# Performance work log

Hardware: AMD Instinct MI355X
Metric: run time of the kernel (lower is better)

## Reference

```python
import jax, jax.numpy as jnp
import numpy as np

B, NCAMS = 1, 6
C_FEAT = 64                     # fusion_feat_in_dim
H, W = 88, 160                  # per-camera feature map size at fusion level
VOX_SIZE = (100, 100, 20)       # (x_dim, y_dim, z_dim) voxel counts
VOX_STR = (-50.0, -50.0, -15.0)
VOX_UNIT = (1.0, 1.0, 1.5)
N_VOX = VOX_SIZE[0] * VOX_SIZE[1] * VOX_SIZE[2]
EPS = 1e-8
V_PRE = 64                      # voxel_pre_dim[0]


def make_voxel_pts(dtype):
    # [B, 4, N]; homogeneous (x, y, z, 1) points, layout [z, y, x] flattened
    xs = jnp.linspace(VOX_STR[0], VOX_STR[0] + VOX_UNIT[0] * (VOX_SIZE[0] - 1), VOX_SIZE[0], dtype=dtype)
    ys = jnp.linspace(VOX_STR[1], VOX_STR[1] + VOX_UNIT[1] * (VOX_SIZE[1] - 1), VOX_SIZE[1], dtype=dtype)
    zs = jnp.linspace(VOX_STR[2], VOX_STR[2] + VOX_UNIT[2] * (VOX_SIZE[2] - 1), VOX_SIZE[2], dtype=dtype)
    zdim, ydim, xdim = VOX_SIZE[2], VOX_SIZE[1], VOX_SIZE[0]
    gx = jnp.broadcast_to(xs[None, None, :], (zdim, ydim, xdim)).reshape(-1)
    gy = jnp.broadcast_to(ys[None, :, None], (zdim, ydim, xdim)).reshape(-1)
    gz = jnp.broadcast_to(zs[:, None, None], (zdim, ydim, xdim)).reshape(-1)
    pts = jnp.stack([gx, gy, gz, jnp.ones_like(gx)], axis=0)  # [4, N]
    return jnp.broadcast_to(pts[None], (B, 4, N_VOX))


def _gather(imgf, iy, ix, Wd):
    # imgf: [BN, C, H*W]; iy/ix: [BN, N] int32 -> [BN, C, N]
    lin = iy * Wd + ix
    return jnp.take_along_axis(imgf, lin[:, None, :], axis=2)


def bilinear_sample(img, gx, gy):
    # grid_sample(mode='bilinear', padding_mode='zeros', align_corners=True)
    BN, C, Hd, Wd = img.shape
    x = (gx + 1.0) * 0.5 * (Wd - 1)
    y = (gy + 1.0) * 0.5 * (Hd - 1)
    x0 = jnp.floor(x); y0 = jnp.floor(y)
    wx1 = x - x0; wx0 = 1.0 - wx1
    wy1 = y - y0; wy0 = 1.0 - wy1
    imgf = img.reshape(BN, C, Hd * Wd)
    out = jnp.zeros((BN, C, gx.shape[1]), dtype=img.dtype)
    for xi, wxi in ((x0, wx0), (x0 + 1.0, wx1)):
        for yi, wyi in ((y0, wy0), (y0 + 1.0, wy1)):
            valid = (xi >= 0) & (xi <= Wd - 1) & (yi >= 0) & (yi <= Hd - 1)
            ii = jnp.clip(xi, 0, Wd - 1).astype(jnp.int32)
            jj = jnp.clip(yi, 0, Hd - 1).astype(jnp.int32)
            w = (wxi * wyi * valid.astype(img.dtype))[:, None, :]
            out = out + _gather(imgf, jj, ii, Wd) * w
    return out


def nearest_sample(img, gx, gy):
    # grid_sample(mode='nearest', padding_mode='zeros', align_corners=True)
    BN, C, Hd, Wd = img.shape
    x = (gx + 1.0) * 0.5 * (Wd - 1)
    y = (gy + 1.0) * 0.5 * (Hd - 1)
    xi = jnp.round(x); yi = jnp.round(y)
    valid = (xi >= 0) & (xi <= Wd - 1) & (yi >= 0) & (yi <= Hd - 1)
    ii = jnp.clip(xi, 0, Wd - 1).astype(jnp.int32)
    jj = jnp.clip(yi, 0, Hd - 1).astype(jnp.int32)
    imgf = img.reshape(BN, C, Hd * Wd)
    return _gather(imgf, jj, ii, Wd) * valid[:, None, :].astype(img.dtype)


def setup_inputs() -> dict:
    key = jax.random.key(0)
    ks = jax.random.split(key, 8)
    return {
        'multi_img_feat': jax.random.normal(ks[0], (B, NCAMS, C_FEAT, H, W), jnp.float32),
        'mask': jax.random.uniform(ks[1], (B, NCAMS, 1, H, W), jnp.float32),
        'K': jax.random.normal(ks[2], (B, NCAMS, 4, 4), jnp.float32),
        'extrinsics': jax.random.normal(ks[3], (B, NCAMS, 4, 4), jnp.float32),
        'w_no': jax.random.normal(ks[4], (V_PRE, C_FEAT + 1), jnp.float32) * 0.05,
        'b_no': jax.random.normal(ks[5], (V_PRE,), jnp.float32) * 0.05,
        'w_o': jax.random.normal(ks[6], (V_PRE, 2 * (C_FEAT + 1)), jnp.float32) * 0.05,
        'b_o': jax.random.normal(ks[7], (V_PRE,), jnp.float32) * 0.05,
    }


def reference(multi_img_feat, mask, K, extrinsics, w_no, b_no, w_o, b_o):
    Bb, NC, C, Hd, Wd = multi_img_feat.shape
    dt = multi_img_feat.dtype
    vpts = make_voxel_pts(dt)                                          # [B,4,N]
    vpts_c = jnp.broadcast_to(vpts[:, None], (Bb, NC, 4, N_VOX)).reshape(Bb * NC, 4, N_VOX)
    feats = multi_img_feat.reshape(Bb * NC, C, Hd, Wd)
    masks = mask.reshape(Bb * NC, 1, Hd, Wd)                           # interp to (H,W) is identity (same size, align_corners)
    ext = extrinsics.reshape(Bb * NC, 4, 4)[:, :3, :]
    K3 = K.reshape(Bb * NC, 4, 4)[:, :3, :3]

    v_local = jnp.einsum('bij,bjn->bin', ext, vpts_c)                  # [BN,3,N]
    cam_pts = jnp.einsum('bij,bjn->bin', K3, v_local)
    pix = cam_pts[:, :2] / (cam_pts[:, 2:3] + EPS)
    pix = jnp.where(jnp.all(jnp.isfinite(pix)), pix, jnp.clip(pix, -Wd * 2.0, Wd * 2.0))
    gx = (pix[:, 0] / (Wd - 1) - 0.5) * 2.0                            # [BN,N] normalized coords
    gy = (pix[:, 1] / (Hd - 1) - 0.5) * 2.0

    feat_w = bilinear_sample(feats, gx, gy)                            # [BN,C,N]
    m_occ = nearest_sample(masks, gx, gy) > 0.5                        # [BN,1,N]
    m_depth = v_local[:, 2:3] > 0
    oob = (gx > 1) | (gx < -1) | (gy > 1) | (gy < -1)
    valid = (m_occ & m_depth & (~oob)[:, None, :]).astype(dt)          # [BN,1,N]

    feat_w = jnp.concatenate([feat_w, v_local[:, 2:3] / VOX_SIZE[0]], axis=1) * valid  # [BN,C+1,N]

    feat_w = feat_w.reshape(Bb, NC, C + 1, N_VOX)
    valid = valid.reshape(Bb, NC, 1, N_VOX)
    count = valid.sum(axis=1)                                          # [B,1,N]

    # non-overlap branch: voxels seen by exactly one camera
    no_mask = (count == 1).astype(dt)
    vox_no = feat_w.sum(axis=1) * no_mask
    vox_no = jax.nn.elu(jnp.einsum('oc,bcn->bon', w_no, vox_no) + b_no[None, :, None]) * no_mask

    # overlap branch: cams {0,3,4} vs {1,2,5}
    o_mask = (count == 2).astype(dt)
    feat1 = feat_w[:, 0] + feat_w[:, 3] + feat_w[:, 4]
    feat2 = feat_w[:, 1] + feat_w[:, 2] + feat_w[:, 5]
    vox_o = jnp.concatenate([feat1, feat2], axis=1)                    # [B,2*(C+1),N]
    vox_o = jax.nn.elu(jnp.einsum('oc,bcn->bon', w_o, vox_o) + b_o[None, :, None]) * o_mask

    return vox_no + vox_o                                              # [B, V_PRE, N]
```

## Files before the change

### kernel.cpp

```cpp
#include <hip/hip_runtime.h>
#include <cmath>

#define NC 6
#define CF 64
#define HH 88
#define WW 160
#define NPIX 14080
#define NVOX 200000
#define VPRE 64
#define VB 128
#define NTH 512
#define NWV 8

typedef unsigned int u32;

__global__ __launch_bounds__(256) void zfill(float4* __restrict__ out, int n4) {
    int i = blockIdx.x * 256 + threadIdx.x;
    int stride = gridDim.x * 256;
    for (; i < n4; i += stride) out[i] = make_float4(0.f, 0.f, 0.f, 0.f);
}

__global__ __launch_bounds__(256) void transpose_feats(const float* __restrict__ in,
                                                       float* __restrict__ out) {
    __shared__ float tile[64 * 65];
    int blk = blockIdx.x;
    int c = blk / 220;
    int p0 = (blk - c * 220) * 64;
    int tid = threadIdx.x;
    int lane = tid & 63;
    int quad = tid >> 6;
    for (int r = quad; r < 64; r += 4)
        tile[r * 65 + lane] = in[(c * 64 + r) * NPIX + p0 + lane];
    __syncthreads();
    for (int r = quad; r < 64; r += 4)
        out[((c * NPIX) + p0 + r) * 64 + lane] = tile[lane * 65 + r];
}

__device__ __forceinline__ float elu1(float x) { return x > 0.0f ? x : expm1f(x); }

__device__ __forceinline__ float gather_bilin(const float* __restrict__ fsrc, int useT,
                                              int lane, int cam, float x, float y) {
    float x0f = floorf(x), y0f = floorf(y);
    float wx1 = x - x0f, wx0 = 1.0f - wx1;
    float wy1 = y - y0f, wy0 = 1.0f - wy1;
    float x1f = x0f + 1.0f, y1f = y0f + 1.0f;
    float bx0 = (x0f >= 0.0f && x0f <= 159.0f) ? 1.0f : 0.0f;
    float bx1 = (x1f >= 0.0f && x1f <= 159.0f) ? 1.0f : 0.0f;
    float by0 = (y0f >= 0.0f && y0f <= 87.0f) ? 1.0f : 0.0f;
    float by1 = (y1f >= 0.0f && y1f <= 87.0f) ? 1.0f : 0.0f;
    int ix0 = (int)fminf(fmaxf(x0f, 0.0f), 159.0f);
    int ix1 = (int)fminf(fmaxf(x1f, 0.0f), 159.0f);
    int iy0 = (int)fminf(fmaxf(y0f, 0.0f), 87.0f);
    int iy1 = (int)fminf(fmaxf(y1f, 0.0f), 87.0f);
    int A = useT ? 64 : 1;
    int Boff = useT ? (cam * NPIX * 64 + lane) : ((cam * 64 + lane) * NPIX);
    float v00 = fsrc[(iy0 * WW + ix0) * A + Boff];
    float v01 = fsrc[(iy1 * WW + ix0) * A + Boff];
    float v10 = fsrc[(iy0 * WW + ix1) * A + Boff];
    float v11 = fsrc[(iy1 * WW + ix1) * A + Boff];
    float fv;
    fv  = (wx0 * wy0 * bx0 * by0) * v00;
    fv += (wx0 * wy1 * bx0 * by1) * v01;
    fv += (wx1 * wy0 * bx1 * by0) * v10;
    fv += (wx1 * wy1 * bx1 * by1) * v11;
    return fv;
}

#define FMA8_STEP(W0,W1,W2,W3,W4,W5,W6,W7,CG,F0,F1,F2,F3) \
    a0 += W0[CG]*F0; a0 += W0[CG+1]*F1; a0 += W0[CG+2]*F2; a0 += W0[CG+3]*F3; \
    a1 += W1[CG]*F0; a1 += W1[CG+1]*F1; a1 += W1[CG+2]*F2; a1 += W1[CG+3]*F3; \
    a2 += W2[CG]*F0; a2 += W2[CG+1]*F1; a2 += W2[CG+2]*F2; a2 += W2[CG+3]*F3; \
    a3 += W3[CG]*F0; a3 += W3[CG+1]*F1; a3 += W3[CG+2]*F2; a3 += W3[CG+3]*F3; \
    a4 += W4[CG]*F0; a4 += W4[CG+1]*F1; a4 += W4[CG+2]*F2; a4 += W4[CG+3]*F3; \
    a5 += W5[CG]*F0; a5 += W5[CG+1]*F1; a5 += W5[CG+2]*F2; a5 += W5[CG+3]*F3; \
    a6 += W6[CG]*F0; a6 += W6[CG+1]*F1; a6 += W6[CG+2]*F2; a6 += W6[CG+3]*F3; \
    a7 += W7[CG]*F0; a7 += W7[CG+1]*F1; a7 += W7[CG+2]*F2; a7 += W7[CG+3]*F3;

__global__ __launch_bounds__(NTH, 4) void vox_main(
    const float* __restrict__ feats,
    const float* __restrict__ featT,
    const float* __restrict__ mask,
    const float* __restrict__ Kg,
    const float* __restrict__ ext,
    const float* __restrict__ wno,
    const float* __restrict__ bno,
    const float* __restrict__ wo,
    const float* __restrict__ bo,
    float* __restrict__ outp,
    int useT)
{
    __shared__ float s_ext[72];
    __shared__ float s_K[54];
    __shared__ __align__(16) float4 s_pair[NC * VB];
    __shared__ float s_F[65 * 66];
    __shared__ u32 s_list1[VB], s_list2[VB];
    __shared__ int s_n1, s_n2;

    int tid = threadIdx.x;
    int lane = tid & 63;
    int wv = tid >> 6;
    int base = blockIdx.x * VB;

    if (tid == 0) { s_n1 = 0; s_n2 = 0; }
    if (tid >= 64 && tid < 136) {
        int i = tid - 64;
        s_ext[i] = ext[(i / 12) * 16 + (i % 12)];
    }
    if (tid >= 192 && tid < 246) {
        int i = tid - 192; int cam = i / 9; int e = i - cam * 9;
        s_K[i] = Kg[cam * 16 + (e / 3) * 4 + (e % 3)];
    }
    __syncthreads();

    for (int p = tid; p < NC * VB; p += NTH) {
        #pragma clang fp contract(off)
        int cam = p >> 7;
        int v = p & (VB - 1);
        int n = base + v;
        if (n < NVOX) {
            int xi = n % 100;
            int t = n / 100;
            int yi = t % 100;
            int zi = t / 100;
            float X = -50.0f + (float)xi;
            float Y = -50.0f + (float)yi;
            float Z = -15.0f + 1.5f * (float)zi;
            const float* E = s_ext + cam * 12;
            const float* Kk = s_K + cam * 9;
            float vl0 = E[0]*X + E[1]*Y + E[2]*Z + E[3];
            float vl1 = E[4]*X + E[5]*Y + E[6]*Z + E[7];
            float vl2 = E[8]*X + E[9]*Y + E[10]*Z + E[11];
            float c0 = Kk[0]*vl0 + Kk[1]*vl1 + Kk[2]*vl2;
            float c1 = Kk[3]*vl0 + Kk[4]*vl1 + Kk[5]*vl2;
            float c2 = Kk[6]*vl0 + Kk[7]*vl1 + Kk[8]*vl2;
            float pz = c2 + 1e-8f;
            float px = c0 / pz;
            float py = c1 / pz;
            float gx = (px / 159.0f - 0.5f) * 2.0f;
            float gy = (py / 87.0f - 0.5f) * 2.0f;
            float x = ((gx + 1.0f) * 0.5f) * 159.0f;
            float y = ((gy + 1.0f) * 0.5f) * 87.0f;
            float xr = rintf(x), yr = rintf(y);
            bool nv = (xr >= 0.0f) && (xr <= 159.0f) && (yr >= 0.0f) && (yr <= 87.0f);
            float mval = 0.0f;
            if (nv) mval = mask[(cam * HH + (int)yr) * WW + (int)xr];
            bool ok = (mval > 0.5f) && (vl2 > 0.0f) &&
                      !((gx > 1.0f) || (gx < -1.0f) || (gy > 1.0f) || (gy < -1.0f));
            s_pair[cam * VB + v] = make_float4(x, y, vl2, ok ? 1.0f : 0.0f);
        } else {
            s_pair[cam * VB + v] = make_float4(0.0f, 0.0f, 0.0f, 0.0f);
        }
    }
    __syncthreads();

    if (tid < VB) {
        int v = tid;
        const float* pw = (const float*)s_pair;
        int cnt = 0, cam0 = 0, cam1 = 0;
        #pragma unroll
        for (int c = 0; c < NC; ++c) {
            float w = pw[(c * VB + v) * 4 + 3];
            if (w != 0.0f) { if (cnt == 0) cam0 = c; else if (cnt == 1) cam1 = c; ++cnt; }
        }
        if (cnt == 1) {
            int s = atomicAdd(&s_n1, 1);
            s_list1[s] = (u32)(v | (cam0 << 8));
        } else if (cnt == 2) {
            int s = atomicAdd(&s_n2, 1);
            s_list2[s] = (u32)(v | (cam0 << 8) | (cam1 << 12));
        }
    }
    __syncthreads();

    int n1 = s_n1, n2 = s_n2;
    const float* fsrc = useT ? featT : feats;
    int wvu = __builtin_amdgcn_readfirstlane(wv);
    int obase = wvu * 8;
    const float* w0n = wno + (obase + 0) * 65;
    const float* w1n = wno + (obase + 1) * 65;
    const float* w2n = wno + (obase + 2) * 65;
    const float* w3n = wno + (obase + 3) * 65;
    const float* w4n = wno + (obase + 4) * 65;
    const float* w5n = wno + (obase + 5) * 65;
    const float* w6n = wno + (obase + 6) * 65;
    const float* w7n = wno + (obase + 7) * 65;
    const float* w0o = wo + (obase + 0) * 130;
    const float* w1o = wo + (obase + 1) * 130;
    const float* w2o = wo + (obase + 2) * 130;
    const float* w3o = wo + (obase + 3) * 130;
    const float* w4o = wo + (obase + 4) * 130;
    const float* w5o = wo + (obase + 5) * 130;
    const float* w6o = wo + (obase + 6) * 130;
    const float* w7o = wo + (obase + 7) * 130;

    for (int t0 = 0; t0 < n1; t0 += 64) {
        int tl = min(64, n1 - t0);
        for (int e = wv; e < tl; e += NWV) {
            u32 ent = s_list1[t0 + e];
            int v = ent & 127, c = (ent >> 8) & 7;
            float4 pd = s_pair[c * VB + v];
            float fv = gather_bilin(fsrc, useT, lane, c, pd.x, pd.y);
            s_F[lane * 66 + e] = fv;
            if (lane == 0) s_F[64 * 66 + e] = pd.z / 100.0f;
        }
        __syncthreads();
        float a0 = bno[obase + 0], a1 = bno[obase + 1], a2 = bno[obase + 2], a3 = bno[obase + 3];
        float a4 = bno[obase + 4], a5 = bno[obase + 5], a6 = bno[obase + 6], a7 = bno[obase + 7];
        for (int cg = 0; cg < 64; cg += 4) {
            float f0 = s_F[(cg + 0) * 66 + lane];
            float f1 = s_F[(cg + 1) * 66 + lane];
            float f2 = s_F[(cg + 2) * 66 + lane];
            float f3 = s_F[(cg + 3) * 66 + lane];
            FMA8_STEP(w0n, w1n, w2n, w3n, w4n, w5n, w6n, w7n, cg, f0, f1, f2, f3)
        }
        float fd = s_F[64 * 66 + lane];
        a0 += w0n[64] * fd; a1 += w1n[64] * fd; a2 += w2n[64] * fd; a3 += w3n[64] * fd;
        a4 += w4n[64] * fd; a5 += w5n[64] * fd; a6 += w6n[64] * fd; a7 += w7n[64] * fd;
        if (lane < tl) {
            size_t col = (size_t)(base + (int)(s_list1[t0 + lane] & 127));
            outp[(size_t)(obase + 0) * NVOX + col] = elu1(a0);
            outp[(size_t)(obase + 1) * NVOX + col] = elu1(a1);
            outp[(size_t)(obase + 2) * NVOX + col] = elu1(a2);
            outp[(size_t)(obase + 3) * NVOX + col] = elu1(a3);
            outp[(size_t)(obase + 4) * NVOX + col] = elu1(a4);
            outp[(size_t)(obase + 5) * NVOX + col] = elu1(a5);
            outp[(size_t)(obase + 6) * NVOX + col] = elu1(a6);
            outp[(size_t)(obase + 7) * NVOX + col] = elu1(a7);
        }
        __syncthreads();
    }

    for (int t0 = 0; t0 < n2; t0 += 64) {
        int tl = min(64, n2 - t0);
        for (int e = wv; e < tl; e += NWV) {
            u32 ent = s_list2[t0 + e];
            int v = ent & 127;
            int c0 = (ent >> 8) & 15, c1 = (ent >> 12) & 15;
            float fg = 0.0f, dd = 0.0f;
            if (!(c0 == 1 || c0 == 2 || c0 == 5)) {
                float4 pd = s_pair[c0 * VB + v];
                fg += gather_bilin(fsrc, useT, lane, c0, pd.x, pd.y);
                dd += pd.z / 100.0f;
            }
            if (!(c1 == 1 || c1 == 2 || c1 == 5)) {
                float4 pd = s_pair[c1 * VB + v];
                fg += gather_bilin(fsrc, useT, lane, c1, pd.x, pd.y);
                dd += pd.z / 100.0f;
            }
            s_F[lane * 66 + e] = fg;
            if (lane == 0) s_F[64 * 66 + e] = dd;
        }
        __syncthreads();
        float a0 = bo[obase + 0], a1 = bo[obase + 1], a2 = bo[obase + 2], a3 = bo[obase + 3];
        float a4 = bo[obase + 4], a5 = bo[obase + 5], a6 = bo[obase + 6], a7 = bo[obase + 7];
        for (int cg = 0; cg < 64; cg += 4) {
            float f0 = s_F[(cg + 0) * 66 + lane];
            float f1 = s_F[(cg + 1) * 66 + lane];
            float f2 = s_F[(cg + 2) * 66 + lane];
            float f3 = s_F[(cg + 3) * 66 + lane];
            FMA8_STEP(w0o, w1o, w2o, w3o, w4o, w5o, w6o, w7o, cg, f0, f1, f2, f3)
        }
        {
            float fd = s_F[64 * 66 + lane];
            a0 += w0o[64] * fd; a1 += w1o[64] * fd; a2 += w2o[64] * fd; a3 += w3o[64] * fd;
            a4 += w4o[64] * fd; a5 += w5o[64] * fd; a6 += w6o[64] * fd; a7 += w7o[64] * fd;
        }
        __syncthreads();
        for (int e = wv; e < tl; e += NWV) {
            u32 ent = s_list2[t0 + e];
            int v = ent & 127;
            int c0 = (ent >> 8) & 15, c1 = (ent >> 12) & 15;
            float fg = 0.0f, dd = 0.0f;
            if (c0 == 1 || c0 == 2 || c0 == 5) {
                float4 pd = s_pair[c0 * VB + v];
                fg += gather_bilin(fsrc, useT, lane, c0, pd.x, pd.y);
                dd += pd.z / 100.0f;
            }
            if (c1 == 1 || c1 == 2 || c1 == 5) {
                float4 pd = s_pair[c1 * VB + v];
                fg += gather_bilin(fsrc, useT, lane, c1, pd.x, pd.y);
                dd += pd.z / 100.0f;
            }
            s_F[lane * 66 + e] = fg;
            if (lane == 0) s_F[64 * 66 + e] = dd;
        }
        __syncthreads();
        for (int cg = 0; cg < 64; cg += 4) {
            float f0 = s_F[(cg + 0) * 66 + lane];
            float f1 = s_F[(cg + 1) * 66 + lane];
            float f2 = s_F[(cg + 2) * 66 + lane];
            float f3 = s_F[(cg + 3) * 66 + lane];
            int cgo = cg + 65;
            FMA8_STEP(w0o, w1o, w2o, w3o, w4o, w5o, w6o, w7o, cgo, f0, f1, f2, f3)
        }
        {
            float fd = s_F[64 * 66 + lane];
            a0 += w0o[129] * fd; a1 += w1o[129] * fd; a2 += w2o[129] * fd; a3 += w3o[129] * fd;
            a4 += w4o[129] * fd; a5 += w5o[129] * fd; a6 += w6o[129] * fd; a7 += w7o[129] * fd;
        }
        if (lane < tl) {
            size_t col = (size_t)(base + (int)(s_list2[t0 + lane] & 127));
            outp[(size_t)(obase + 0) * NVOX + col] = elu1(a0);
            outp[(size_t)(obase + 1) * NVOX + col] = elu1(a1);
            outp[(size_t)(obase + 2) * NVOX + col] = elu1(a2);
            outp[(size_t)(obase + 3) * NVOX + col] = elu1(a3);
            outp[(size_t)(obase + 4) * NVOX + col] = elu1(a4);
            outp[(size_t)(obase + 5) * NVOX + col] = elu1(a5);
            outp[(size_t)(obase + 6) * NVOX + col] = elu1(a6);
            outp[(size_t)(obase + 7) * NVOX + col] = elu1(a7);
        }
        __syncthreads();
    }
}

extern "C" void kernel_launch(void* const* d_in, const int* in_sizes, int n_in,
                              void* d_out, int out_size, void* d_ws, size_t ws_size,
                              hipStream_t stream) {
    const float* feats = (const float*)d_in[0];
    const float* mask  = (const float*)d_in[1];
    const float* Kg    = (const float*)d_in[2];
    const float* ext   = (const float*)d_in[3];
    const float* wno   = (const float*)d_in[4];
    const float* bno   = (const float*)d_in[5];
    const float* wo    = (const float*)d_in[6];
    const float* bo    = (const float*)d_in[7];
    float* outp = (float*)d_out;
    float* featT = (float*)d_ws;

    int n4 = out_size / 4;
    zfill<<<2048, 256, 0, stream>>>((float4*)d_out, n4);

    size_t need = (size_t)NC * CF * NPIX * sizeof(float);
    int useT = (ws_size >= need) ? 1 : 0;
    if (useT) {
        transpose_feats<<<NC * 220, 256, 0, stream>>>(feats, featT);
    }
    int nblk = (NVOX + VB - 1) / VB;
    vox_main<<<nblk, NTH, 0, stream>>>(feats, featT, mask, Kg, ext,
                                       wno, bno, wo, bo, outp, useT);
}
```

Measured before the change: 165.8 us.

## Split voxel kernel into geometry compaction pass and dense matvec pass

Adds a prep kernel that projects voxels, classifies them by camera count, and compacts the single-camera and two-camera voxels into global record lists using atomic counters. A second persistent kernel then processes full 64-voxel tiles of these lists for the gather and matvec, so tiles are no longer mostly empty as they were with per-block sparse voxels. This costs an extra launch and a round trip of records through the workspace. The new path is taken only when the workspace is large enough, otherwise the old fused kernel is used.

Measured after the change: 187.8 us. +13.3%, slower.

```diff
diff --git a/kernel.cpp b/kernel.cpp
--- a/kernel.cpp
+++ b/kernel.cpp
@@ -14,10 +14,20 @@
 
 typedef unsigned int u32;
 
-__global__ __launch_bounds__(256) void zfill(float4* __restrict__ out, int n4) {
+#define FEATT_BYTES  (6u * 64u * 14080u * 4u)
+#define REC1_OFF     FEATT_BYTES
+#define REC1_BYTES   (200000u * 16u)
+#define REC2_OFF     (REC1_OFF + REC1_BYTES)
+#define REC2_BYTES   (200000u * 16u)
+#define CNT_OFF      (REC2_OFF + REC2_BYTES)
+#define WS_NEED      (CNT_OFF + 16u)
+
+__global__ __launch_bounds__(256) void zfill(float4* __restrict__ out, int n4,
+                                             int* __restrict__ cnt) {
     int i = blockIdx.x * 256 + threadIdx.x;
     int stride = gridDim.x * 256;
     for (; i < n4; i += stride) out[i] = make_float4(0.f, 0.f, 0.f, 0.f);
+    if (cnt && blockIdx.x == 0 && threadIdx.x < 2) cnt[threadIdx.x] = 0;
 }
 
 __global__ __launch_bounds__(256) void transpose_feats(const float* __restrict__ in,
@@ -76,6 +86,284 @@
     a6 += W6[CG]*F0; a6 += W6[CG+1]*F1; a6 += W6[CG+2]*F2; a6 += W6[CG+3]*F3; \
     a7 += W7[CG]*F0; a7 += W7[CG+1]*F1; a7 += W7[CG+2]*F2; a7 += W7[CG+3]*F3;
 
+#define GEOMETRY_PHASE(SPAIR)                                                  \
+    for (int p = tid; p < NC * VB; p += NTH) {                                 \
+        _Pragma("clang fp contract(off)")                                      \
+        int cam = p >> 7;                                                      \
+        int v = p & (VB - 1);                                                  \
+        int n = base + v;                                                      \
+        if (n < NVOX) {                                                        \
+            int xi = n % 100;                                                  \
+            int t = n / 100;                                                   \
+            int yi = t % 100;                                                  \
+            int zi = t / 100;                                                  \
+            float X = -50.0f + (float)xi;                                      \
+            float Y = -50.0f + (float)yi;                                      \
+            float Z = -15.0f + 1.5f * (float)zi;                               \
+            const float* E = s_ext + cam * 12;                                 \
+            const float* Kk = s_K + cam * 9;                                   \
+            float vl0 = E[0]*X + E[1]*Y + E[2]*Z + E[3];                       \
+            float vl1 = E[4]*X + E[5]*Y + E[6]*Z + E[7];                       \
+            float vl2 = E[8]*X + E[9]*Y + E[10]*Z + E[11];                     \
+            float c0 = Kk[0]*vl0 + Kk[1]*vl1 + Kk[2]*vl2;                      \
+            float c1 = Kk[3]*vl0 + Kk[4]*vl1 + Kk[5]*vl2;                      \
+            float c2 = Kk[6]*vl0 + Kk[7]*vl1 + Kk[8]*vl2;                      \
+            float pz = c2 + 1e-8f;                                             \
+            float px = c0 / pz;                                                \
+            float py = c1 / pz;                                                \
+            float gx = (px / 159.0f - 0.5f) * 2.0f;                            \
+            float gy = (py / 87.0f - 0.5f) * 2.0f;                             \
+            float x = ((gx + 1.0f) * 0.5f) * 159.0f;                           \
+            float y = ((gy + 1.0f) * 0.5f) * 87.0f;                            \
+            float xr = rintf(x), yr = rintf(y);                                \
+            bool nv = (xr >= 0.0f) && (xr <= 159.0f) && (yr >= 0.0f) && (yr <= 87.0f); \
+            float mval = 0.0f;                                                 \
+            if (nv) mval = mask[(cam * HH + (int)yr) * WW + (int)xr];          \
+            bool ok = (mval > 0.5f) && (vl2 > 0.0f) &&                         \
+                      !((gx > 1.0f) || (gx < -1.0f) || (gy > 1.0f) || (gy < -1.0f)); \
+            SPAIR[cam * VB + v] = make_float4(x, y, vl2, ok ? 1.0f : 0.0f);    \
+        } else {                                                               \
+            SPAIR[cam * VB + v] = make_float4(0.0f, 0.0f, 0.0f, 0.0f);         \
+        }                                                                      \
+    }
+
+__global__ __launch_bounds__(NTH) void vox_prep(
+    const float* __restrict__ mask,
+    const float* __restrict__ Kg,
+    const float* __restrict__ ext,
+    float4* __restrict__ rec1,
+    float4* __restrict__ rec2,
+    int* __restrict__ cnt)
+{
+    __shared__ float s_ext[72];
+    __shared__ float s_K[54];
+    __shared__ __align__(16) float4 s_pair[NC * VB];
+    __shared__ u32 s_list1[VB], s_list2[VB];
+    __shared__ int s_n1, s_n2, s_base1, s_base2;
+
+    int tid = threadIdx.x;
+    int base = blockIdx.x * VB;
+
+    if (tid == 0) { s_n1 = 0; s_n2 = 0; }
+    if (tid >= 64 && tid < 136) {
+        int i = tid - 64;
+        s_ext[i] = ext[(i / 12) * 16 + (i % 12)];
+    }
+    if (tid >= 192 && tid < 246) {
+        int i = tid - 192; int cam = i / 9; int e = i - cam * 9;
+        s_K[i] = Kg[cam * 16 + (e / 3) * 4 + (e % 3)];
+    }
+    __syncthreads();
+
+    GEOMETRY_PHASE(s_pair)
+    __syncthreads();
+
+    if (tid < VB) {
+        int v = tid;
+        const float* pw = (const float*)s_pair;
+        int cnt_ = 0, cam0 = 0, cam1 = 0;
+        #pragma unroll
+        for (int c = 0; c < NC; ++c) {
+            float w = pw[(c * VB + v) * 4 + 3];
+            if (w != 0.0f) { if (cnt_ == 0) cam0 = c; else if (cnt_ == 1) cam1 = c; ++cnt_; }
+        }
+        if (cnt_ == 1) {
+            int s = atomicAdd(&s_n1, 1);
+            s_list1[s] = (u32)(v | (cam0 << 8));
+        } else if (cnt_ == 2) {
+            int s = atomicAdd(&s_n2, 1);
+            s_list2[s] = (u32)(v | (cam0 << 8) | (cam1 << 12));
+        }
+    }
+    __syncthreads();
+    if (tid == 0) s_base1 = atomicAdd(&cnt[0], s_n1);
+    if (tid == 1) s_base2 = atomicAdd(&cnt[1], s_n2);
+    __syncthreads();
+
+    int n1 = s_n1, n2 = s_n2;
+    if (tid < n1) {
+        u32 ent = s_list1[tid];
+        int v = ent & 127, c = (ent >> 8) & 7;
+        float4 pd = s_pair[c * VB + v];
+        int meta = ((base + v) << 3) | c;
+        rec1[s_base1 + tid] = make_float4(pd.x, pd.y, pd.z, __int_as_float(meta));
+    }
+    if (tid >= 256 && tid - 256 < n2) {
+        int j = tid - 256;
+        u32 ent = s_list2[j];
+        int v = ent & 127;
+        int c0 = (ent >> 8) & 15, c1 = (ent >> 12) & 15;
+        float4 p0 = s_pair[c0 * VB + v];
+        float4 p1 = s_pair[c1 * VB + v];
+        int vox = base + v;
+        rec2[2 * (s_base2 + j) + 0] = make_float4(p0.x, p0.y, p0.z, __int_as_float((vox << 3) | c0));
+        rec2[2 * (s_base2 + j) + 1] = make_float4(p1.x, p1.y, p1.z, __int_as_float((vox << 3) | c1));
+    }
+}
+
+__global__ __launch_bounds__(NTH) void vox_mv(
+    const float* __restrict__ feats,
+    const float* __restrict__ featT,
+    const float4* __restrict__ rec1,
+    const float4* __restrict__ rec2,
+    const int* __restrict__ cnt,
+    const float* __restrict__ wno,
+    const float* __restrict__ bno,
+    const float* __restrict__ wo,
+    const float* __restrict__ bo,
+    float* __restrict__ outp,
+    int useT)
+{
+    __shared__ float s_F[65 * 66];
+    __shared__ int s_vox[64];
+
+    int tid = threadIdx.x;
+    int lane = tid & 63;
+    int wv = tid >> 6;
+    int c1 = cnt[0], c2 = cnt[1];
+    int nt1 = (c1 + 63) >> 6, nt2 = (c2 + 63) >> 6;
+    int nt = nt1 + nt2;
+
+    const float* fsrc = useT ? featT : feats;
+    int wvu = __builtin_amdgcn_readfirstlane(wv);
+    int obase = wvu * 8;
+    const float* w0n = wno + (obase + 0) * 65;
+    const float* w1n = wno + (obase + 1) * 65;
+    const float* w2n = wno + (obase + 2) * 65;
+    const float* w3n = wno + (obase + 3) * 65;
+    const float* w4n = wno + (obase + 4) * 65;
+    const float* w5n = wno + (obase + 5) * 65;
+    const float* w6n = wno + (obase + 6) * 65;
+    const float* w7n = wno + (obase + 7) * 65;
+    const float* w0o = wo + (obase + 0) * 130;
+    const float* w1o = wo + (obase + 1) * 130;
+    const float* w2o = wo + (obase + 2) * 130;
+    const float* w3o = wo + (obase + 3) * 130;
+    const float* w4o = wo + (obase + 4) * 130;
+    const float* w5o = wo + (obase + 5) * 130;
+    const float* w6o = wo + (obase + 6) * 130;
+    const float* w7o = wo + (obase + 7) * 130;
+
+    for (int t = blockIdx.x; t < nt; t += gridDim.x) {
+        if (t < nt1) {
+            int e0 = t << 6;
+            int tl = min(64, c1 - e0);
+            for (int e = wv; e < tl; e += NWV) {
+                float4 r = rec1[e0 + e];
+                int meta = __float_as_int(r.w);
+                int cam = meta & 7;
+                float fv = gather_bilin(fsrc, useT, lane, cam, r.x, r.y);
+                s_F[lane * 66 + e] = fv;
+                if (lane == 0) { s_F[64 * 66 + e] = r.z / 100.0f; s_vox[e] = meta >> 3; }
+            }
+            __syncthreads();
+            float a0 = bno[obase + 0], a1 = bno[obase + 1], a2 = bno[obase + 2], a3 = bno[obase + 3];
+            float a4 = bno[obase + 4], a5 = bno[obase + 5], a6 = bno[obase + 6], a7 = bno[obase + 7];
+            for (int cg = 0; cg < 64; cg += 4) {
+                float f0 = s_F[(cg + 0) * 66 + lane];
+                float f1 = s_F[(cg + 1) * 66 + lane];
+                float f2 = s_F[(cg + 2) * 66 + lane];
+                float f3 = s_F[(cg + 3) * 66 + lane];
+                FMA8_STEP(w0n, w1n, w2n, w3n, w4n, w5n, w6n, w7n, cg, f0, f1, f2, f3)
+            }
+            float fd = s_F[64 * 66 + lane];
+            a0 += w0n[64] * fd; a1 += w1n[64] * fd; a2 += w2n[64] * fd; a3 += w3n[64] * fd;
+            a4 += w4n[64] * fd; a5 += w5n[64] * fd; a6 += w6n[64] * fd; a7 += w7n[64] * fd;
+            if (lane < tl) {
+                size_t col = (size_t)s_vox[lane];
+                outp[(size_t)(obase + 0) * NVOX + col] = elu1(a0);
+                outp[(size_t)(obase + 1) * NVOX + col] = elu1(a1);
+                outp[(size_t)(obase + 2) * NVOX + col] = elu1(a2);
+                outp[(size_t)(obase + 3) * NVOX + col] = elu1(a3);
+                outp[(size_t)(obase + 4) * NVOX + col] = elu1(a4);
+                outp[(size_t)(obase + 5) * NVOX + col] = elu1(a5);
+                outp[(size_t)(obase + 6) * NVOX + col] = elu1(a6);
+                outp[(size_t)(obase + 7) * NVOX + col] = elu1(a7);
+            }
+            __syncthreads();
+        } else {
+            int e0 = (t - nt1) << 6;
+            int tl = min(64, c2 - e0);
+            for (int e = wv; e < tl; e += NWV) {
+                float4 r0 = rec2[2 * (e0 + e) + 0];
+                float4 r1 = rec2[2 * (e0 + e) + 1];
+                int m0 = __float_as_int(r0.w), m1 = __float_as_int(r1.w);
+                int ca = m0 & 7, cb = m1 & 7;
+                float fg = 0.0f, dd = 0.0f;
+                if (!(ca == 1 || ca == 2 || ca == 5)) {
+                    fg += gather_bilin(fsrc, useT, lane, ca, r0.x, r0.y);
+                    dd += r0.z / 100.0f;
+                }
+                if (!(cb == 1 || cb == 2 || cb == 5)) {
+                    fg += gather_bilin(fsrc, useT, lane, cb, r1.x, r1.y);
+                    dd += r1.z / 100.0f;
+                }
+                s_F[lane * 66 + e] = fg;
+                if (lane == 0) { s_F[64 * 66 + e] = dd; s_vox[e] = m0 >> 3; }
+            }
+            __syncthreads();
+            float a0 = bo[obase + 0], a1 = bo[obase + 1], a2 = bo[obase + 2], a3 = bo[obase + 3];
+            float a4 = bo[obase + 4], a5 = bo[obase + 5], a6 = bo[obase + 6], a7 = bo[obase + 7];
+            for (int cg = 0; cg < 64; cg += 4) {
+                float f0 = s_F[(cg + 0) * 66 + lane];
+                float f1 = s_F[(cg + 1) * 66 + lane];
+                float f2 = s_F[(cg + 2) * 66 + lane];
+                float f3 = s_F[(cg + 3) * 66 + lane];
+                FMA8_STEP(w0o, w1o, w2o, w3o, w4o, w5o, w6o, w7o, cg, f0, f1, f2, f3)
+            }
+            {
+                float fd = s_F[64 * 66 + lane];
+                a0 += w0o[64] * fd; a1 += w1o[64] * fd; a2 += w2o[64] * fd; a3 += w3o[64] * fd;
+                a4 += w4o[64] * fd; a5 += w5o[64] * fd; a6 += w6o[64] * fd; a7 += w7o[64] * fd;
+            }
+            __syncthreads();
+            for (int e = wv; e < tl; e += NWV) {
+                float4 r0 = rec2[2 * (e0 + e) + 0];
+                float4 r1 = rec2[2 * (e0 + e) + 1];
+                int m0 = __float_as_int(r0.w), m1 = __float_as_int(r1.w);
+                int ca = m0 & 7, cb = m1 & 7;
+                float fg = 0.0f, dd = 0.0f;
+                if (ca == 1 || ca == 2 || ca == 5) {
+                    fg += gather_bilin(fsrc, useT, lane, ca, r0.x, r0.y);
+                    dd += r0.z / 100.0f;
+                }
+                if (cb == 1 || cb == 2 || cb == 5) {
+                    fg += gather_bilin(fsrc, useT, lane, cb, r1.x, r1.y);
+                    dd += r1.z / 100.0f;
+                }
+                s_F[lane * 66 + e] = fg;
+                if (lane == 0) s_F[64 * 66 + e] = dd;
+            }
+            __syncthreads();
+            for (int cg = 0; cg < 64; cg += 4) {
+                float f0 = s_F[(cg + 0) * 66 + lane];
+                float f1 = s_F[(cg + 1) * 66 + lane];
+                float f2 = s_F[(cg + 2) * 66 + lane];
+                float f3 = s_F[(cg + 3) * 66 + lane];
+                int cgo = cg + 65;
+                FMA8_STEP(w0o, w1o, w2o, w3o, w4o, w5o, w6o, w7o, cgo, f0, f1, f2, f3)
+            }
+            {
+                float fd = s_F[64 * 66 + lane];
+                a0 += w0o[129] * fd; a1 += w1o[129] * fd; a2 += w2o[129] * fd; a3 += w3o[129] * fd;
+                a4 += w4o[129] * fd; a5 += w5o[129] * fd; a6 += w6o[129] * fd; a7 += w7o[129] * fd;
+            }
+            if (lane < tl) {
+                size_t col = (size_t)s_vox[lane];
+                outp[(size_t)(obase + 0) * NVOX + col] = elu1(a0);
+                outp[(size_t)(obase + 1) * NVOX + col] = elu1(a1);
+                outp[(size_t)(obase + 2) * NVOX + col] = elu1(a2);
+                outp[(size_t)(obase + 3) * NVOX + col] = elu1(a3);
+                outp[(size_t)(obase + 4) * NVOX + col] = elu1(a4);
+                outp[(size_t)(obase + 5) * NVOX + col] = elu1(a5);
+                outp[(size_t)(obase + 6) * NVOX + col] = elu1(a6);
+                outp[(size_t)(obase + 7) * NVOX + col] = elu1(a7);
+            }
+            __syncthreads();
+        }
+    }
+}
+
 __global__ __launch_bounds__(NTH, 4) void vox_main(
     const float* __restrict__ feats,
     const float* __restrict__ featT,
@@ -112,45 +400,7 @@
     }
     __syncthreads();
 
-    for (int p = tid; p < NC * VB; p += NTH) {
-        #pragma clang fp contract(off)
-        int cam = p >> 7;
-        int v = p & (VB - 1);
-        int n = base + v;
-        if (n < NVOX) {
-            int xi = n % 100;
-            int t = n / 100;
-            int yi = t % 100;
-            int zi = t / 100;
-            float X = -50.0f + (float)xi;
-            float Y = -50.0f + (float)yi;
-            float Z = -15.0f + 1.5f * (float)zi;
-            const float* E = s_ext + cam * 12;
-            const float* Kk = s_K + cam * 9;
-            float vl0 = E[0]*X + E[1]*Y + E[2]*Z + E[3];
-            float vl1 = E[4]*X + E[5]*Y + E[6]*Z + E[7];
-            float vl2 = E[8]*X + E[9]*Y + E[10]*Z + E[11];
-            float c0 = Kk[0]*vl0 + Kk[1]*vl1 + Kk[2]*vl2;
-            float c1 = Kk[3]*vl0 + Kk[4]*vl1 + Kk[5]*vl2;
-            float c2 = Kk[6]*vl0 + Kk[7]*vl1 + Kk[8]*vl2;
-            float pz = c2 + 1e-8f;
-            float px = c0 / pz;
-            float py = c1 / pz;
-            float gx = (px / 159.0f - 0.5f) * 2.0f;
-            float gy = (py / 87.0f - 0.5f) * 2.0f;
-            float x = ((gx + 1.0f) * 0.5f) * 159.0f;
-            float y = ((gy + 1.0f) * 0.5f) * 87.0f;
-            float xr = rintf(x), yr = rintf(y);
-            bool nv = (xr >= 0.0f) && (xr <= 159.0f) && (yr >= 0.0f) && (yr <= 87.0f);
-            float mval = 0.0f;
-            if (nv) mval = mask[(cam * HH + (int)yr) * WW + (int)xr];
-            bool ok = (mval > 0.5f) && (vl2 > 0.0f) &&
-                      !((gx > 1.0f) || (gx < -1.0f) || (gy > 1.0f) || (gy < -1.0f));
-            s_pair[cam * VB + v] = make_float4(x, y, vl2, ok ? 1.0f : 0.0f);
-        } else {
-            s_pair[cam * VB + v] = make_float4(0.0f, 0.0f, 0.0f, 0.0f);
-        }
-    }
+    GEOMETRY_PHASE(s_pair)
     __syncthreads();
 
     if (tid < VB) {
@@ -325,17 +575,27 @@
     const float* wo    = (const float*)d_in[6];
     const float* bo    = (const float*)d_in[7];
     float* outp = (float*)d_out;
-    float* featT = (float*)d_ws;
-
+    char* wsb = (char*)d_ws;
+    float* featT = (float*)wsb;
+
+    int useT = (ws_size >= (size_t)FEATT_BYTES) ? 1 : 0;
+    int full = (ws_size >= (size_t)WS_NEED) ? 1 : 0;
+    int nblk = (NVOX + VB - 1) / VB;
     int n4 = out_size / 4;
-    zfill<<<2048, 256, 0, stream>>>((float4*)d_out, n4);
-
-    size_t need = (size_t)NC * CF * NPIX * sizeof(float);
-    int useT = (ws_size >= need) ? 1 : 0;
-    if (useT) {
+
+    if (full) {
+        float4* rec1 = (float4*)(wsb + REC1_OFF);
+        float4* rec2 = (float4*)(wsb + REC2_OFF);
+        int* cnt = (int*)(wsb + CNT_OFF);
+        zfill<<<2048, 256, 0, stream>>>((float4*)d_out, n4, cnt);
         transpose_feats<<<NC * 220, 256, 0, stream>>>(feats, featT);
-    }
-    int nblk = (NVOX + VB - 1) / VB;
-    vox_main<<<nblk, NTH, 0, stream>>>(feats, featT, mask, Kg, ext,
-                                       wno, bno, wo, bo, outp, useT);
+        vox_prep<<<nblk, NTH, 0, stream>>>(mask, Kg, ext, rec1, rec2, cnt);
+        vox_mv<<<1024, NTH, 0, stream>>>(feats, featT, rec1, rec2, cnt,
+                                         wno, bno, wo, bo, outp, useT);
+    } else {
+        zfill<<<2048, 256, 0, stream>>>((float4*)d_out, n4, (int*)nullptr);
+        if (useT) transpose_feats<<<NC * 220, 256, 0, stream>>>(feats, featT);
+        vox_main<<<nblk, NTH, 0, stream>>>(feats, featT, mask, Kg, ext,
+                                           wno, bno, wo, bo, outp, useT);
+    }
 }
```

## Fuse output zero-fill into voxel kernel and compact per-voxel records with larger blocks

Applied to the files above, without the earlier changes.

The separate zero-fill kernel is removed, and each voxel block now zeroes its own output slice at the start. Voxel blocks grow from 128 to 512, so one thread handles one voxel and loops over all six cameras in registers. The shared per-camera pair table is replaced by compacted float4 records carrying sample coordinates, depth and packed voxel/camera metadata. This drops a kernel launch and a full output write pass, and cuts shared-memory traffic, at the cost of fewer blocks and a changed launch-bounds occupancy hint. The vectorised zeroing assumes the per-block voxel count is a multiple of four, which holds for 200000/512.

Measured after the change: 177.8 us. +7.2%, slower.

```diff
diff --git a/kernel.cpp b/kernel.cpp
--- a/kernel.cpp
+++ b/kernel.cpp
@@ -8,17 +8,13 @@
 #define NPIX 14080
 #define NVOX 200000
 #define VPRE 64
-#define VB 128
+#define VB 512
 #define NTH 512
 #define NWV 8
 
 typedef unsigned int u32;
 
-__global__ __launch_bounds__(256) void zfill(float4* __restrict__ out, int n4) {
-    int i = blockIdx.x * 256 + threadIdx.x;
-    int stride = gridDim.x * 256;
-    for (; i < n4; i += stride) out[i] = make_float4(0.f, 0.f, 0.f, 0.f);
-}
+#define FEATT_BYTES  (6u * 64u * 14080u * 4u)
 
 __global__ __launch_bounds__(256) void transpose_feats(const float* __restrict__ in,
                                                        float* __restrict__ out) {
@@ -76,7 +72,7 @@
     a6 += W6[CG]*F0; a6 += W6[CG+1]*F1; a6 += W6[CG+2]*F2; a6 += W6[CG+3]*F3; \
     a7 += W7[CG]*F0; a7 += W7[CG+1]*F1; a7 += W7[CG+2]*F2; a7 += W7[CG+3]*F3;
 
-__global__ __launch_bounds__(NTH, 4) void vox_main(
+__global__ __launch_bounds__(NTH) void vox_fused(
     const float* __restrict__ feats,
     const float* __restrict__ featT,
     const float* __restrict__ mask,
@@ -91,15 +87,17 @@
 {
     __shared__ float s_ext[72];
     __shared__ float s_K[54];
-    __shared__ __align__(16) float4 s_pair[NC * VB];
     __shared__ float s_F[65 * 66];
-    __shared__ u32 s_list1[VB], s_list2[VB];
+    __shared__ __align__(16) float4 s_rec1[VB];
+    __shared__ __align__(16) float4 s_rec2[2 * VB];
+    __shared__ int s_vox[64];
     __shared__ int s_n1, s_n2;
 
     int tid = threadIdx.x;
     int lane = tid & 63;
     int wv = tid >> 6;
     int base = blockIdx.x * VB;
+    int vlim = min(VB, NVOX - base);
 
     if (tid == 0) { s_n1 = 0; s_n2 = 0; }
     if (tid >= 64 && tid < 136) {
@@ -110,21 +108,32 @@
         int i = tid - 192; int cam = i / 9; int e = i - cam * 9;
         s_K[i] = Kg[cam * 16 + (e / 3) * 4 + (e % 3)];
     }
+
+    {
+        int ng4 = vlim >> 2;
+        for (int i = tid; i < 64 * 128; i += NTH) {
+            int r = i >> 7, cg = i & 127;
+            if (cg < ng4)
+                *(float4*)(outp + (size_t)r * NVOX + base + (cg << 2)) =
+                    make_float4(0.f, 0.f, 0.f, 0.f);
+        }
+    }
     __syncthreads();
 
-    for (int p = tid; p < NC * VB; p += NTH) {
+    if (tid < vlim) {
         #pragma clang fp contract(off)
-        int cam = p >> 7;
-        int v = p & (VB - 1);
-        int n = base + v;
-        if (n < NVOX) {
-            int xi = n % 100;
-            int t = n / 100;
-            int yi = t % 100;
-            int zi = t / 100;
-            float X = -50.0f + (float)xi;
-            float Y = -50.0f + (float)yi;
-            float Z = -15.0f + 1.5f * (float)zi;
+        int n = base + tid;
+        int xi = n % 100;
+        int t = n / 100;
+        int yi = t % 100;
+        int zi = t / 100;
+        float X = -50.0f + (float)xi;
+        float Y = -50.0f + (float)yi;
+        float Z = -15.0f + 1.5f * (float)zi;
+        int cnt = 0, cam0 = 0, cam1 = 0;
+        float ax = 0.f, ay = 0.f, az = 0.f, bx = 0.f, by = 0.f, bz = 0.f;
+        #pragma unroll
+        for (int cam = 0; cam < NC; ++cam) {
             const float* E = s_ext + cam * 12;
             const float* Kk = s_K + cam * 9;
             float vl0 = E[0]*X + E[1]*Y + E[2]*Z + E[3];
@@ -146,28 +155,19 @@
             if (nv) mval = mask[(cam * HH + (int)yr) * WW + (int)xr];
             bool ok = (mval > 0.5f) && (vl2 > 0.0f) &&
                       !((gx > 1.0f) || (gx < -1.0f) || (gy > 1.0f) || (gy < -1.0f));
-            s_pair[cam * VB + v] = make_float4(x, y, vl2, ok ? 1.0f : 0.0f);
-        } else {
-            s_pair[cam * VB + v] = make_float4(0.0f, 0.0f, 0.0f, 0.0f);
-        }
-    }
-    __syncthreads();
-
-    if (tid < VB) {
-        int v = tid;
-        const float* pw = (const float*)s_pair;
-        int cnt = 0, cam0 = 0, cam1 = 0;
-        #pragma unroll
-        for (int c = 0; c < NC; ++c) {
-            float w = pw[(c * VB + v) * 4 + 3];
-            if (w != 0.0f) { if (cnt == 0) cam0 = c; else if (cnt == 1) cam1 = c; ++cnt; }
+            if (ok) {
+                if (cnt == 0) { ax = x; ay = y; az = vl2; cam0 = cam; }
+                else if (cnt == 1) { bx = x; by = y; bz = vl2; cam1 = cam; }
+                ++cnt;
+            }
         }
         if (cnt == 1) {
             int s = atomicAdd(&s_n1, 1);
-            s_list1[s] = (u32)(v | (cam0 << 8));
+            s_rec1[s] = make_float4(ax, ay, az, __int_as_float((n << 3) | cam0));
         } else if (cnt == 2) {
             int s = atomicAdd(&s_n2, 1);
-            s_list2[s] = (u32)(v | (cam0 << 8) | (cam1 << 12));
+            s_rec2[2 * s + 0] = make_float4(ax, ay, az, __int_as_float((n << 3) | cam0));
+            s_rec2[2 * s + 1] = make_float4(bx, by, bz, __int_as_float((n << 3) | cam1));
         }
     }
     __syncthreads();
@@ -196,12 +196,12 @@
     for (int t0 = 0; t0 < n1; t0 += 64) {
         int tl = min(64, n1 - t0);
         for (int e = wv; e < tl; e += NWV) {
-            u32 ent = s_list1[t0 + e];
-            int v = ent & 127, c = (ent >> 8) & 7;
-            float4 pd = s_pair[c * VB + v];
-            float fv = gather_bilin(fsrc, useT, lane, c, pd.x, pd.y);
+            float4 r = s_rec1[t0 + e];
+            int meta = __float_as_int(r.w);
+            int cam = meta & 7;
+            float fv = gather_bilin(fsrc, useT, lane, cam, r.x, r.y);
             s_F[lane * 66 + e] = fv;
-            if (lane == 0) s_F[64 * 66 + e] = pd.z / 100.0f;
+            if (lane == 0) { s_F[64 * 66 + e] = r.z / 100.0f; s_vox[e] = meta >> 3; }
         }
         __syncthreads();
         float a0 = bno[obase + 0], a1 = bno[obase + 1], a2 = bno[obase + 2], a3 = bno[obase + 3];
@@ -217,7 +217,7 @@
         a0 += w0n[64] * fd; a1 += w1n[64] * fd; a2 += w2n[64] * fd; a3 += w3n[64] * fd;
         a4 += w4n[64] * fd; a5 += w5n[64] * fd; a6 += w6n[64] * fd; a7 += w7n[64] * fd;
         if (lane < tl) {
-            size_t col = (size_t)(base + (int)(s_list1[t0 + lane] & 127));
+            size_t col = (size_t)s_vox[lane];
             outp[(size_t)(obase + 0) * NVOX + col] = elu1(a0);
             outp[(size_t)(obase + 1) * NVOX + col] = elu1(a1);
             outp[(size_t)(obase + 2) * NVOX + col] = elu1(a2);
@@ -233,22 +233,21 @@
     for (int t0 = 0; t0 < n2; t0 += 64) {
         int tl = min(64, n2 - t0);
         for (int e = wv; e < tl; e += NWV) {
-            u32 ent = s_list2[t0 + e];
-            int v = ent & 127;
-            int c0 = (ent >> 8) & 15, c1 = (ent >> 12) & 15;
+            float4 r0 = s_rec2[2 * (t0 + e) + 0];
+            float4 r1 = s_rec2[2 * (t0 + e) + 1];
+            int m0 = __float_as_int(r0.w), m1 = __float_as_int(r1.w);
+            int ca = m0 & 7, cb = m1 & 7;
             float fg = 0.0f, dd = 0.0f;
-            if (!(c0 == 1 || c0 == 2 || c0 == 5)) {
-                float4 pd = s_pair[c0 * VB + v];
-                fg += gather_bilin(fsrc, useT, lane, c0, pd.x, pd.y);
-                dd += pd.z / 100.0f;
-            }
-            if (!(c1 == 1 || c1 == 2 || c1 == 5)) {
-                float4 pd = s_pair[c1 * VB + v];
-                fg += gather_bilin(fsrc, useT, lane, c1, pd.x, pd.y);
-                dd += pd.z / 100.0f;
+            if (!(ca == 1 || ca == 2 || ca == 5)) {
+                fg += gather_bilin(fsrc, useT, lane, ca, r0.x, r0.y);
+                dd += r0.z / 100.0f;
+            }
+            if (!(cb == 1 || cb == 2 || cb == 5)) {
+                fg += gather_bilin(fsrc, useT, lane, cb, r1.x, r1.y);
+                dd += r1.z / 100.0f;
             }
             s_F[lane * 66 + e] = fg;
-            if (lane == 0) s_F[64 * 66 + e] = dd;
+            if (lane == 0) { s_F[64 * 66 + e] = dd; s_vox[e] = m0 >> 3; }
         }
         __syncthreads();
         float a0 = bo[obase + 0], a1 = bo[obase + 1], a2 = bo[obase + 2], a3 = bo[obase + 3];
@@ -267,19 +266,18 @@
         }
         __syncthreads();
         for (int e = wv; e < tl; e += NWV) {
-            u32 ent = s_list2[t0 + e];
-            int v = ent & 127;
-            int c0 = (ent >> 8) & 15, c1 = (ent >> 12) & 15;
+            float4 r0 = s_rec2[2 * (t0 + e) + 0];
+            float4 r1 = s_rec2[2 * (t0 + e) + 1];
+            int m0 = __float_as_int(r0.w), m1 = __float_as_int(r1.w);
+            int ca = m0 & 7, cb = m1 & 7;
             float fg = 0.0f, dd = 0.0f;
-            if (c0 == 1 || c0 == 2 || c0 == 5) {
-                float4 pd = s_pair[c0 * VB + v];
-                fg += gather_bilin(fsrc, useT, lane, c0, pd.x, pd.y);
-                dd += pd.z / 100.0f;
-            }
-            if (c1 == 1 || c1 == 2 || c1 == 5) {
-                float4 pd = s_pair[c1 * VB + v];
-                fg += gather_bilin(fsrc, useT, lane, c1, pd.x, pd.y);
-                dd += pd.z / 100.0f;
+            if (ca == 1 || ca == 2 || ca == 5) {
+                fg += gather_bilin(fsrc, useT, lane, ca, r0.x, r0.y);
+                dd += r0.z / 100.0f;
+            }
+            if (cb == 1 || cb == 2 || cb == 5) {
+                fg += gather_bilin(fsrc, useT, lane, cb, r1.x, r1.y);
+                dd += r1.z / 100.0f;
             }
             s_F[lane * 66 + e] = fg;
             if (lane == 0) s_F[64 * 66 + e] = dd;
@@ -299,7 +297,7 @@
             a4 += w4o[129] * fd; a5 += w5o[129] * fd; a6 += w6o[129] * fd; a7 += w7o[129] * fd;
         }
         if (lane < tl) {
-            size_t col = (size_t)(base + (int)(s_list2[t0 + lane] & 127));
+            size_t col = (size_t)s_vox[lane];
             outp[(size_t)(obase + 0) * NVOX + col] = elu1(a0);
             outp[(size_t)(obase + 1) * NVOX + col] = elu1(a1);
             outp[(size_t)(obase + 2) * NVOX + col] = elu1(a2);
@@ -327,15 +325,11 @@
     float* outp = (float*)d_out;
     float* featT = (float*)d_ws;
 
-    int n4 = out_size / 4;
-    zfill<<<2048, 256, 0, stream>>>((float4*)d_out, n4);
-
-    size_t need = (size_t)NC * CF * NPIX * sizeof(float);
-    int useT = (ws_size >= need) ? 1 : 0;
+    int useT = (ws_size >= (size_t)FEATT_BYTES) ? 1 : 0;
     if (useT) {
         transpose_feats<<<NC * 220, 256, 0, stream>>>(feats, featT);
     }
     int nblk = (NVOX + VB - 1) / VB;
-    vox_main<<<nblk, NTH, 0, stream>>>(feats, featT, mask, Kg, ext,
-                                       wno, bno, wo, bo, outp, useT);
+    vox_fused<<<nblk, NTH, 0, stream>>>(feats, featT, mask, Kg, ext,
+                                        wno, bno, wo, bo, outp, useT);
 }
```
